# Kernel optimization log

Hardware: AMD Instinct MI355X
Metric: run time of the kernel (lower is better)

The kernel has to match this reference:

```python
import jax, jax.numpy as jnp
import numpy as np

EPS = 1e-6  # cell eps
LN_EPS = 1e-5  # torch LayerNorm default


def layer_norm(x, gamma, beta):
    mu = jnp.mean(x, axis=-1, keepdims=True)
    var = jnp.mean(jnp.square(x - mu), axis=-1, keepdims=True)
    return (x - mu) * jax.lax.rsqrt(var + LN_EPS) * gamma + beta


def normalized_exp_gate(pre):
    centered = pre - jnp.mean(pre, axis=1, keepdims=True)
    e = jnp.exp(jnp.clip(centered, -5.0, 5.0))
    return e / (jnp.sum(e, axis=1, keepdims=True) + EPS)


def setup_inputs() -> dict:
    key = jax.random.key(0)
    B, Din, H = 8192, 512, 1024
    ks = jax.random.split(key, 16)
    std = 1.0 / np.sqrt(H)
    u = lambda k, shape: jax.random.uniform(k, shape, jnp.float32, -std, std)
    return {
        "x": jax.random.normal(ks[0], (B, Din), jnp.float32),
        "h_prev": jax.random.normal(ks[1], (B, H), jnp.float32),
        "c_prev": jax.random.normal(ks[2], (B, H), jnp.float32),
        "Wx": u(ks[3], (4 * H, Din)),
        "bx": u(ks[4], (4 * H,)),
        "Wh": u(ks[5], (4 * H, H)),
        "bh": u(ks[6], (4 * H,)),
        "ln_in_g": u(ks[7], (4 * H,)),
        "ln_in_b": u(ks[8], (4 * H,)),
        "ln_hu_g": u(ks[9], (4 * H,)),
        "ln_hu_b": u(ks[10], (4 * H,)),
        "ln_c_g": u(ks[11], (H,)),
        "ln_c_b": u(ks[12], (H,)),
        "ln_h_g": u(ks[13], (H,)),
        "ln_h_b": u(ks[14], (H,)),
    }


def reference(x, h_prev, c_prev, Wx, bx, Wh, bh,
              ln_in_g, ln_in_b, ln_hu_g, ln_hu_b,
              ln_c_g, ln_c_b, ln_h_g, ln_h_b):
    # dropout p=0 -> identity (eval mode)
    gates_x = layer_norm(x @ Wx.T + bx, ln_in_g, ln_in_b)      # [B, 4H]
    gates_h = layer_norm(h_prev @ Wh.T + bh, ln_hu_g, ln_hu_b)  # [B, 4H]
    gates = gates_x + gates_h
    i, f, g, o = jnp.split(gates, 4, axis=1)
    i = normalized_exp_gate(i)
    f = normalized_exp_gate(f)
    gate_sum = i + f
    i = i / (gate_sum + EPS)
    f = f / (gate_sum + EPS)
    c_tilde = jnp.tanh(g)
    c = layer_norm(f * c_prev + i * c_tilde, ln_c_g, ln_c_b)
    o = jax.nn.sigmoid(o)
    c_out = layer_norm(jnp.tanh(c), ln_h_g, ln_h_b)
    h = o * c_out
    return (h, c)
```

## Files before the change

### kernel.cpp

```cpp
#include <hip/hip_runtime.h>
#include <hip/hip_bf16.h>
#include <stdint.h>
#include <math.h>

#define EPS_CELL 1e-6f
#define LN_EPS   1e-5f

typedef short short8 __attribute__((ext_vector_type(8)));
typedef float f32x4 __attribute__((ext_vector_type(4)));
typedef unsigned short ushort;

__device__ __forceinline__ ushort f2bf(float f) {
    union { float f; uint32_t u; } v; v.f = f;
    uint32_t r = v.u + 0x7FFFu + ((v.u >> 16) & 1u);
    return (ushort)(r >> 16);
}
__device__ __forceinline__ float bfbits2f(uint32_t hi16_in_place) {
    union { uint32_t u; float f; } v; v.u = hi16_in_place;
    return v.f;
}

__device__ __forceinline__ float fexp(float x)  { return __builtin_amdgcn_exp2f(x * 1.4426950408889634f); }
__device__ __forceinline__ float frcp(float x)  { return __builtin_amdgcn_rcpf(x); }
__device__ __forceinline__ float frsq(float x)  { return __builtin_amdgcn_rsqf(x); }
__device__ __forceinline__ float ftanh(float x) {
    float xc = fminf(fmaxf(x, -15.f), 15.f);
    float t  = fexp(2.f * xc);
    return (t - 1.f) * frcp(t + 1.f);
}
__device__ __forceinline__ float fsigm(float x) { return frcp(1.f + fexp(-x)); }

__global__ __launch_bounds__(256) void cast_all(
        const float* __restrict__ x,  const float* __restrict__ h,
        const float* __restrict__ wx, const float* __restrict__ wh,
        ushort* __restrict__ xb, ushort* __restrict__ hb,
        ushort* __restrict__ wxb, ushort* __restrict__ whb) {
    long i = ((long)blockIdx.x * 256 + threadIdx.x) * 8;
    const float* src; ushort* dst; long off;
    if      (i <  4194304L) { src = x;  dst = xb;  off = i; }
    else if (i < 12582912L) { src = h;  dst = hb;  off = i - 4194304L; }
    else if (i < 14680064L) { src = wx; dst = wxb; off = i - 12582912L; }
    else                    { src = wh; dst = whb; off = i - 14680064L; }
    const float4* p = (const float4*)(src + off);
    float4 a = p[0], b = p[1];
    uint4 r;
    r.x = (uint32_t)f2bf(a.x) | ((uint32_t)f2bf(a.y) << 16);
    r.y = (uint32_t)f2bf(a.z) | ((uint32_t)f2bf(a.w) << 16);
    r.z = (uint32_t)f2bf(b.x) | ((uint32_t)f2bf(b.y) << 16);
    r.w = (uint32_t)f2bf(b.z) | ((uint32_t)f2bf(b.w) << 16);
    *(uint4*)(dst + off) = r;
}

#define BAR()        __builtin_amdgcn_s_barrier()
#define SPRIO(x)     __builtin_amdgcn_s_setprio(x)
#define WAIT_LGKM0() do { asm volatile("s_waitcnt lgkmcnt(0)" ::: "memory"); \
                          __builtin_amdgcn_sched_barrier(0); } while (0)
#define WAIT_VM6()   do { asm volatile("s_waitcnt vmcnt(6)" ::: "memory"); \
                          __builtin_amdgcn_sched_barrier(0); } while (0)
#define WAIT_VM0()   do { asm volatile("s_waitcnt vmcnt(0)" ::: "memory"); \
                          __builtin_amdgcn_sched_barrier(0); } while (0)

template<int K>
__global__ __launch_bounds__(512, 2) void gemm256_8ph(
        const ushort* __restrict__ Ag,
        const ushort* __restrict__ Bg,
        const float*  __restrict__ bias,
        ushort* __restrict__ C,
        int GN, int m_base) {
    constexpr int NT = K / 64;
    constexpr int NP = NT / 2;

    __shared__ ushort lds[65536];

    const int t    = threadIdx.x;
    const int lane = t & 63;
    const int w    = t >> 6;
    const int wr   = w >> 2;
    const int wc   = w & 3;
    const int ln   = lane & 15;
    const int hi   = lane >> 4;
    const int sx   = ln & 7;

    const int bid = blockIdx.x;
    const int cpx = gridDim.x >> 3;
    const int wg  = (bid & 7) * cpx + (bid >> 3);
    const int n0  = (wg & 15) * 256;
    const int m0  = (wg >> 4) * 256 + m_base;

    const int trow = t >> 3;
    const int scol = (((t & 7) ^ (trow & 7)) * 8);

#define STG_A(buf, j, kb) __builtin_amdgcn_global_load_lds( \
    (const __attribute__((address_space(1))) void*)(Ag + (size_t)(m0 + (j)*64 + trow) * K + (kb) + scol), \
    (__attribute__((address_space(3))) void*)(lds + (buf)*32768 + (j)*4096 + t*8), 16, 0, 0)
#define STG_B(buf, j, kb) __builtin_amdgcn_global_load_lds( \
    (const __attribute__((address_space(1))) void*)(Bg + (size_t)(n0 + (j)*64 + trow) * K + (kb) + scol), \
    (__attribute__((address_space(3))) void*)(lds + (buf)*32768 + 16384 + (j)*4096 + t*8), 16, 0, 0)

    const int ca0  = ((0 + hi) ^ sx) * 8;
    const int ca1  = ((4 + hi) ^ sx) * 8;
    const int arow = (wr * 16 + ln) * 64;
    const int brow = (wc * 16 + ln) * 64 + 16384;

    short8 af[2][4], bf0[2][2], bf1[2][2];
    f32x4  acc[8][4] = {};

#define LD_A(buf, mbase) do { _Pragma("unroll") for (int m = 0; m < 4; ++m) { \
    af[0][m] = *(const short8*)&lds[(buf)*32768 + arow + ((mbase)+m)*2048 + ca0]; \
    af[1][m] = *(const short8*)&lds[(buf)*32768 + arow + ((mbase)+m)*2048 + ca1]; } } while (0)
#define LD_B(dst, buf, nbase) do { _Pragma("unroll") for (int n = 0; n < 2; ++n) { \
    dst[0][n] = *(const short8*)&lds[(buf)*32768 + brow + ((nbase)+n)*4096 + ca0]; \
    dst[1][n] = *(const short8*)&lds[(buf)*32768 + brow + ((nbase)+n)*4096 + ca1]; } } while (0)
#define MMQ(mb, nb, B_) do { _Pragma("unroll") for (int kk = 0; kk < 2; ++kk) \
    _Pragma("unroll") for (int m = 0; m < 4; ++m) \
    _Pragma("unroll") for (int n = 0; n < 2; ++n) \
        acc[(mb)+m][(nb)+n] = __builtin_amdgcn_mfma_f32_16x16x32_bf16( \
            af[kk][m], B_[kk][n], acc[(mb)+m][(nb)+n], 0, 0, 0); } while (0)

    STG_B(0,0,0);  STG_B(0,1,0);
    STG_A(0,0,0);  STG_A(0,1,0);
    STG_B(0,2,0);  STG_B(0,3,0);
    STG_A(0,2,0);  STG_A(0,3,0);
    STG_B(1,0,64); STG_B(1,1,64);
    STG_A(1,0,64); STG_A(1,1,64);
    STG_B(1,2,64); STG_B(1,3,64);
    WAIT_VM6(); BAR();

    for (int p = 0; p < NP; ++p) {
        const int k1 = (2*p + 1) * 64;
        const int t2 = (2*p + 2 < NT) ? (2*p + 2) : (2*p);
        const int t3 = (2*p + 3 < NT) ? (2*p + 3) : (2*p + 1);
        const int k2 = t2 * 64, k3 = t3 * 64;

        LD_A(0, 0); LD_B(bf0, 0, 0);
        STG_A(1,2,k1); STG_A(1,3,k1);
        BAR(); WAIT_LGKM0();
        SPRIO(1); MMQ(0,0,bf0); SPRIO(0); BAR();
        LD_B(bf1, 0, 2);
        STG_B(0,0,k2); STG_B(0,1,k2);
        BAR(); WAIT_LGKM0();
        SPRIO(1); MMQ(0,2,bf1); SPRIO(0); BAR();
        LD_A(0, 4);
        STG_A(0,0,k2); STG_A(0,1,k2);
        BAR(); WAIT_LGKM0();
        SPRIO(1); MMQ(4,0,bf0); SPRIO(0); BAR();
        STG_B(0,2,k2); STG_B(0,3,k2);
        BAR();
        SPRIO(1); MMQ(4,2,bf1); SPRIO(0);
        WAIT_VM6(); BAR();
        LD_A(1, 0); LD_B(bf0, 1, 0);
        STG_A(0,2,k2); STG_A(0,3,k2);
        BAR(); WAIT_LGKM0();
        SPRIO(1); MMQ(0,0,bf0); SPRIO(0); BAR();
        LD_B(bf1, 1, 2);
        STG_B(1,0,k3); STG_B(1,1,k3);
        BAR(); WAIT_LGKM0();
        SPRIO(1); MMQ(0,2,bf1); SPRIO(0); BAR();
        LD_A(1, 4);
        STG_A(1,0,k3); STG_A(1,1,k3);
        BAR(); WAIT_LGKM0();
        SPRIO(1); MMQ(4,0,bf0); SPRIO(0); BAR();
        STG_B(1,2,k3); STG_B(1,3,k3);
        BAR();
        SPRIO(1); MMQ(4,2,bf1); SPRIO(0);
        WAIT_VM6(); BAR();
    }

    WAIT_VM0();
    BAR();
#pragma unroll
    for (int n = 0; n < 4; ++n) {
        int cl   = n * 64 + wc * 16 + ln;
        float bv = bias[n0 + cl];
#pragma unroll
        for (int m = 0; m < 8; ++m) {
#pragma unroll
            for (int r = 0; r < 4; ++r) {
                int row = m * 32 + wr * 16 + hi * 4 + r;
                int sc  = (cl & 7) + ((((cl >> 3) ^ (row & 7))) << 3);
                lds[row * 256 + sc] = f2bf(acc[m][n][r] + bv);
            }
        }
    }
    BAR();
    {
        const int rr = t >> 5;
        const int oc = (t & 31) * 8;
#pragma unroll
        for (int i = 0; i < 16; ++i) {
            int row = i * 16 + rr;
            int sc  = (((oc >> 3) ^ (row & 7)) << 3);
            uint4 vv = *(const uint4*)&lds[row * 256 + sc];
            *(uint4*)(C + (size_t)(m0 + row) * GN + n0 + oc) = vv;
        }
    }
#undef STG_A
#undef STG_B
#undef LD_A
#undef LD_B
#undef MMQ
}

template<int NV>
__device__ __forceinline__ void reduce2(float* v0, float* v1, float* s0, float* s1) {
    const int lane = threadIdx.x & 63;
    const int w    = threadIdx.x >> 6;
#pragma unroll
    for (int i = 0; i < NV; ++i) {
        float a = v0[i], b = v1[i];
#pragma unroll
        for (int m = 32; m > 0; m >>= 1) {
            a += __shfl_xor(a, m, 64);
            b += __shfl_xor(b, m, 64);
        }
        if (lane == 0) { s0[i * 4 + w] = a; s1[i * 4 + w] = b; }
    }
    __syncthreads();
#pragma unroll
    for (int i = 0; i < NV; ++i) {
        v0[i] = s0[i * 4 + 0] + s0[i * 4 + 1] + s0[i * 4 + 2] + s0[i * 4 + 3];
        v1[i] = s1[i * 4 + 0] + s1[i * 4 + 1] + s1[i * 4 + 2] + s1[i * 4 + 3];
    }
}

__global__ __launch_bounds__(256) void fused_cell2(
        const ushort* __restrict__ U, const ushort* __restrict__ V,
        const float* __restrict__ c_prev,
        const float* __restrict__ g_in, const float* __restrict__ b_in,
        const float* __restrict__ g_hu, const float* __restrict__ b_hu,
        const float* __restrict__ g_c,  const float* __restrict__ b_c,
        const float* __restrict__ g_h,  const float* __restrict__ b_h,
        float* __restrict__ out_h, float* __restrict__ out_c) {
    __shared__ float sred[2][4][16];
    const int t  = threadIdx.x;
    const int c0 = t * 4;
    const int rb = blockIdx.x * 2;

    uint2 uu[2][4], vv[2][4];
    float4 cp4[2];
#pragma unroll
    for (int rj = 0; rj < 2; ++rj) {
        const size_t rowG = (size_t)(rb + rj) * 4096;
#pragma unroll
        for (int q = 0; q < 4; ++q) {
            uu[rj][q] = *(const uint2*)(U + rowG + q * 1024 + c0);
            vv[rj][q] = *(const uint2*)(V + rowG + q * 1024 + c0);
        }
        cp4[rj] = *(const float4*)(c_prev + (size_t)(rb + rj) * 1024 + c0);
    }
    float4 gc4 = *(const float4*)(g_c + c0);
    float4 bc4 = *(const float4*)(b_c + c0);
    float4 gh4 = *(const float4*)(g_h + c0);
    float4 bh4 = *(const float4*)(b_h + c0);

    float red0[4] = {0.f, 0.f, 0.f, 0.f};
    float red1[4] = {0.f, 0.f, 0.f, 0.f};
#pragma unroll
    for (int rj = 0; rj < 2; ++rj) {
        float* rd = rj ? red1 : red0;
#pragma unroll
        for (int q = 0; q < 4; ++q) {
            float u0 = bfbits2f(uu[rj][q].x << 16), u1 = bfbits2f(uu[rj][q].x & 0xFFFF0000u);
            float u2 = bfbits2f(uu[rj][q].y << 16), u3 = bfbits2f(uu[rj][q].y & 0xFFFF0000u);
            float v0 = bfbits2f(vv[rj][q].x << 16), v1 = bfbits2f(vv[rj][q].x & 0xFFFF0000u);
            float v2 = bfbits2f(vv[rj][q].y << 16), v3 = bfbits2f(vv[rj][q].y & 0xFFFF0000u);
            rd[0] += u0 + u1 + u2 + u3;
            rd[1] += u0 * u0 + u1 * u1 + u2 * u2 + u3 * u3;
            rd[2] += v0 + v1 + v2 + v3;
            rd[3] += v0 * v0 + v1 * v1 + v2 * v2 + v3 * v3;
        }
    }
    reduce2<4>(red0, red1, sred[0][0], sred[1][0]);
    const float inv4096 = 1.f / 4096.f;
    float mu_u[2], rs_u[2], mu_v[2], rs_v[2];
    mu_u[0] = red0[0] * inv4096; mu_v[0] = red0[2] * inv4096;
    rs_u[0] = frsq(red0[1] * inv4096 - mu_u[0] * mu_u[0] + LN_EPS);
    rs_v[0] = frsq(red0[3] * inv4096 - mu_v[0] * mu_v[0] + LN_EPS);
    mu_u[1] = red1[0] * inv4096; mu_v[1] = red1[2] * inv4096;
    rs_u[1] = frsq(red1[1] * inv4096 - mu_u[1] * mu_u[1] + LN_EPS);
    rs_v[1] = frsq(red1[3] * inv4096 - mu_v[1] * mu_v[1] + LN_EPS);

    float gate[2][4][4];
#pragma unroll
    for (int q = 0; q < 4; ++q) {
        const int idx = q * 1024 + c0;
        float4 ga = *(const float4*)(g_in + idx);
        float4 ba = *(const float4*)(b_in + idx);
        float4 gb = *(const float4*)(g_hu + idx);
        float4 bb = *(const float4*)(b_hu + idx);
        float gaa[4] = {ga.x, ga.y, ga.z, ga.w};
        float baa[4] = {ba.x, ba.y, ba.z, ba.w};
        float gba[4] = {gb.x, gb.y, gb.z, gb.w};
        float bba[4] = {bb.x, bb.y, bb.z, bb.w};
#pragma unroll
        for (int rj = 0; rj < 2; ++rj) {
            float uf[4], vf[4];
            uf[0] = bfbits2f(uu[rj][q].x << 16); uf[1] = bfbits2f(uu[rj][q].x & 0xFFFF0000u);
            uf[2] = bfbits2f(uu[rj][q].y << 16); uf[3] = bfbits2f(uu[rj][q].y & 0xFFFF0000u);
            vf[0] = bfbits2f(vv[rj][q].x << 16); vf[1] = bfbits2f(vv[rj][q].x & 0xFFFF0000u);
            vf[2] = bfbits2f(vv[rj][q].y << 16); vf[3] = bfbits2f(vv[rj][q].y & 0xFFFF0000u);
#pragma unroll
            for (int j = 0; j < 4; ++j) {
                float zu = (uf[j] - mu_u[rj]) * rs_u[rj];
                float zv = (vf[j] - mu_v[rj]) * rs_v[rj];
                gate[rj][q][j] = zu * gaa[j] + baa[j] + zv * gba[j] + bba[j];
            }
        }
    }

    float ei[2][4], ef[2][4];
    red0[0] = red0[1] = red1[0] = red1[1] = 0.f;
#pragma unroll
    for (int rj = 0; rj < 2; ++rj) {
        float* rd = rj ? red1 : red0;
#pragma unroll
        for (int q = 0; q < 4; ++q) {
            ei[rj][q] = fexp(fminf(fmaxf(gate[rj][0][q], -20.f), 20.f));
            ef[rj][q] = fexp(fminf(fmaxf(gate[rj][1][q], -20.f), 20.f));
            rd[0] += ei[rj][q]; rd[1] += ef[rj][q];
        }
    }
    reduce2<2>(red0, red1, sred[0][1], sred[1][1]);
    float inv_si[2], inv_sf[2];
    inv_si[0] = frcp(red0[0] + EPS_CELL); inv_sf[0] = frcp(red0[1] + EPS_CELL);
    inv_si[1] = frcp(red1[0] + EPS_CELL); inv_sf[1] = frcp(red1[1] + EPS_CELL);

    float cpv[2][4];
    red0[0] = red0[1] = red1[0] = red1[1] = 0.f;
#pragma unroll
    for (int rj = 0; rj < 2; ++rj) {
        float* rd = rj ? red1 : red0;
        float cpr[4] = {cp4[rj].x, cp4[rj].y, cp4[rj].z, cp4[rj].w};
#pragma unroll
        for (int q = 0; q < 4; ++q) {
            float in_ = ei[rj][q] * inv_si[rj];
            float fn_ = ef[rj][q] * inv_sf[rj];
            float den = frcp(in_ + fn_ + EPS_CELL);
            cpv[rj][q] = fn_ * den * cpr[q] + in_ * den * ftanh(gate[rj][2][q]);
            rd[0] += cpv[rj][q]; rd[1] += cpv[rj][q] * cpv[rj][q];
        }
    }
    reduce2<2>(red0, red1, sred[0][2], sred[1][2]);
    const float inv1024 = 1.f / 1024.f;
    float mu_c[2], rs_c[2];
    mu_c[0] = red0[0] * inv1024;
    rs_c[0] = frsq(red0[1] * inv1024 - mu_c[0] * mu_c[0] + LN_EPS);
    mu_c[1] = red1[0] * inv1024;
    rs_c[1] = frsq(red1[1] * inv1024 - mu_c[1] * mu_c[1] + LN_EPS);

    float th[2][4];
    {
        float gca[4] = {gc4.x, gc4.y, gc4.z, gc4.w};
        float bca[4] = {bc4.x, bc4.y, bc4.z, bc4.w};
        red0[0] = red0[1] = red1[0] = red1[1] = 0.f;
#pragma unroll
        for (int rj = 0; rj < 2; ++rj) {
            float* rd = rj ? red1 : red0;
            float cv[4];
#pragma unroll
            for (int q = 0; q < 4; ++q) {
                cv[q] = (cpv[rj][q] - mu_c[rj]) * rs_c[rj] * gca[q] + bca[q];
                th[rj][q] = ftanh(cv[q]);
                rd[0] += th[rj][q]; rd[1] += th[rj][q] * th[rj][q];
            }
            float4 o; o.x = cv[0]; o.y = cv[1]; o.z = cv[2]; o.w = cv[3];
            *(float4*)(out_c + (size_t)(rb + rj) * 1024 + c0) = o;
        }
    }
    reduce2<2>(red0, red1, sred[0][3], sred[1][3]);
    float mu_t[2], rs_t[2];
    mu_t[0] = red0[0] * inv1024;
    rs_t[0] = frsq(red0[1] * inv1024 - mu_t[0] * mu_t[0] + LN_EPS);
    mu_t[1] = red1[0] * inv1024;
    rs_t[1] = frsq(red1[1] * inv1024 - mu_t[1] * mu_t[1] + LN_EPS);

    {
        float gha[4] = {gh4.x, gh4.y, gh4.z, gh4.w};
        float bha[4] = {bh4.x, bh4.y, bh4.z, bh4.w};
#pragma unroll
        for (int rj = 0; rj < 2; ++rj) {
            float hv[4];
#pragma unroll
            for (int q = 0; q < 4; ++q) {
                float co = (th[rj][q] - mu_t[rj]) * rs_t[rj] * gha[q] + bha[q];
                hv[q] = fsigm(gate[rj][3][q]) * co;
            }
            float4 o; o.x = hv[0]; o.y = hv[1]; o.z = hv[2]; o.w = hv[3];
            *(float4*)(out_h + (size_t)(rb + rj) * 1024 + c0) = o;
        }
    }
}

extern "C" void kernel_launch(void* const* d_in, const int* in_sizes, int n_in,
                              void* d_out, int out_size, void* d_ws, size_t ws_size,
                              hipStream_t stream) {
    const float* x       = (const float*)d_in[0];
    const float* h_prev  = (const float*)d_in[1];
    const float* c_prev  = (const float*)d_in[2];
    const float* Wx      = (const float*)d_in[3];
    const float* bx      = (const float*)d_in[4];
    const float* Wh      = (const float*)d_in[5];
    const float* bh      = (const float*)d_in[6];
    const float* ln_in_g = (const float*)d_in[7];
    const float* ln_in_b = (const float*)d_in[8];
    const float* ln_hu_g = (const float*)d_in[9];
    const float* ln_hu_b = (const float*)d_in[10];
    const float* ln_c_g  = (const float*)d_in[11];
    const float* ln_c_b  = (const float*)d_in[12];
    const float* ln_h_g  = (const float*)d_in[13];
    const float* ln_h_b  = (const float*)d_in[14];

    const int B = 8192, Din = 512, H = 1024, G = 4096;

    ushort* xb  = (ushort*)d_ws;
    ushort* hb  = xb  + (size_t)B * Din;
    ushort* wxb = hb  + (size_t)B * H;
    ushort* whb = wxb + (size_t)G * Din;
    ushort* U   = whb + (size_t)G * H;
    ushort* V   = U   + (size_t)B * G;

    cast_all<<<9216, 256, 0, stream>>>(x, h_prev, Wx, Wh, xb, hb, wxb, whb);

    gemm256_8ph<512> <<<dim3(256), 512, 0, stream>>>(xb, wxb, bx, U, G, 0);
    gemm256_8ph<512> <<<dim3(256), 512, 0, stream>>>(xb, wxb, bx, U, G, 4096);
    gemm256_8ph<1024><<<dim3(256), 512, 0, stream>>>(hb, whb, bh, V, G, 0);
    gemm256_8ph<1024><<<dim3(256), 512, 0, stream>>>(hb, whb, bh, V, G, 4096);

    float* out_h = (float*)d_out;
    float* out_c = out_h + (size_t)B * H;
    fused_cell2<<<B / 2, 256, 0, stream>>>(U, V, c_prev,
                                           ln_in_g, ln_in_b, ln_hu_g, ln_hu_b,
                                           ln_c_g, ln_c_b, ln_h_g, ln_h_b,
                                           out_h, out_c);
}
```

Before: 213.9 us.

## Make fused cell kernel persistent over row pairs with register double-buffered prefetch

The fused LayerNorm/gate kernel now has each block process four consecutive row pairs instead of one. It loads the next pair's U, V and c_prev values into a second register buffer while the current pair is computed. The aim is to hide global-memory latency behind the reduction and transcendental work, and to load the per-column LN parameters once per block. In exchange the kernel uses more registers, which may lower occupancy, and the grid shrinks from 4096 blocks to 1024.

```diff
diff --git a/kernel.cpp b/kernel.cpp
--- a/kernel.cpp
+++ b/kernel.cpp
@@ -223,7 +223,7 @@
     }
 }
 
-__global__ __launch_bounds__(256) void fused_cell2(
+__global__ __launch_bounds__(256) void fused_cell_p(
         const ushort* __restrict__ U, const ushort* __restrict__ V,
         const float* __restrict__ c_prev,
         const float* __restrict__ g_in, const float* __restrict__ b_in,
@@ -234,159 +234,181 @@
     __shared__ float sred[2][4][16];
     const int t  = threadIdx.x;
     const int c0 = t * 4;
-    const int rb = blockIdx.x * 2;
-
-    uint2 uu[2][4], vv[2][4];
-    float4 cp4[2];
+    const int pb = blockIdx.x * 4;
+
+    const float4 gc4 = *(const float4*)(g_c + c0);
+    const float4 bc4 = *(const float4*)(b_c + c0);
+    const float4 gh4 = *(const float4*)(g_h + c0);
+    const float4 bh4 = *(const float4*)(b_h + c0);
+
+    uint2 uu[2][2][4], vv[2][2][4];
+    float4 cp[2][2];
+
 #pragma unroll
     for (int rj = 0; rj < 2; ++rj) {
-        const size_t rowG = (size_t)(rb + rj) * 4096;
+        const size_t rowG = (size_t)(2 * pb + rj) * 4096;
 #pragma unroll
         for (int q = 0; q < 4; ++q) {
-            uu[rj][q] = *(const uint2*)(U + rowG + q * 1024 + c0);
-            vv[rj][q] = *(const uint2*)(V + rowG + q * 1024 + c0);
-        }
-        cp4[rj] = *(const float4*)(c_prev + (size_t)(rb + rj) * 1024 + c0);
-    }
-    float4 gc4 = *(const float4*)(g_c + c0);
-    float4 bc4 = *(const float4*)(b_c + c0);
-    float4 gh4 = *(const float4*)(g_h + c0);
-    float4 bh4 = *(const float4*)(b_h + c0);
-
-    float red0[4] = {0.f, 0.f, 0.f, 0.f};
-    float red1[4] = {0.f, 0.f, 0.f, 0.f};
-#pragma unroll
-    for (int rj = 0; rj < 2; ++rj) {
-        float* rd = rj ? red1 : red0;
-#pragma unroll
-        for (int q = 0; q < 4; ++q) {
-            float u0 = bfbits2f(uu[rj][q].x << 16), u1 = bfbits2f(uu[rj][q].x & 0xFFFF0000u);
-            float u2 = bfbits2f(uu[rj][q].y << 16), u3 = bfbits2f(uu[rj][q].y & 0xFFFF0000u);
-            float v0 = bfbits2f(vv[rj][q].x << 16), v1 = bfbits2f(vv[rj][q].x & 0xFFFF0000u);
-            float v2 = bfbits2f(vv[rj][q].y << 16), v3 = bfbits2f(vv[rj][q].y & 0xFFFF0000u);
-            rd[0] += u0 + u1 + u2 + u3;
-            rd[1] += u0 * u0 + u1 * u1 + u2 * u2 + u3 * u3;
-            rd[2] += v0 + v1 + v2 + v3;
-            rd[3] += v0 * v0 + v1 * v1 + v2 * v2 + v3 * v3;
-        }
-    }
-    reduce2<4>(red0, red1, sred[0][0], sred[1][0]);
-    const float inv4096 = 1.f / 4096.f;
-    float mu_u[2], rs_u[2], mu_v[2], rs_v[2];
-    mu_u[0] = red0[0] * inv4096; mu_v[0] = red0[2] * inv4096;
-    rs_u[0] = frsq(red0[1] * inv4096 - mu_u[0] * mu_u[0] + LN_EPS);
-    rs_v[0] = frsq(red0[3] * inv4096 - mu_v[0] * mu_v[0] + LN_EPS);
-    mu_u[1] = red1[0] * inv4096; mu_v[1] = red1[2] * inv4096;
-    rs_u[1] = frsq(red1[1] * inv4096 - mu_u[1] * mu_u[1] + LN_EPS);
-    rs_v[1] = frsq(red1[3] * inv4096 - mu_v[1] * mu_v[1] + LN_EPS);
-
-    float gate[2][4][4];
-#pragma unroll
-    for (int q = 0; q < 4; ++q) {
-        const int idx = q * 1024 + c0;
-        float4 ga = *(const float4*)(g_in + idx);
-        float4 ba = *(const float4*)(b_in + idx);
-        float4 gb = *(const float4*)(g_hu + idx);
-        float4 bb = *(const float4*)(b_hu + idx);
-        float gaa[4] = {ga.x, ga.y, ga.z, ga.w};
-        float baa[4] = {ba.x, ba.y, ba.z, ba.w};
-        float gba[4] = {gb.x, gb.y, gb.z, gb.w};
-        float bba[4] = {bb.x, bb.y, bb.z, bb.w};
-#pragma unroll
-        for (int rj = 0; rj < 2; ++rj) {
-            float uf[4], vf[4];
-            uf[0] = bfbits2f(uu[rj][q].x << 16); uf[1] = bfbits2f(uu[rj][q].x & 0xFFFF0000u);
-            uf[2] = bfbits2f(uu[rj][q].y << 16); uf[3] = bfbits2f(uu[rj][q].y & 0xFFFF0000u);
-            vf[0] = bfbits2f(vv[rj][q].x << 16); vf[1] = bfbits2f(vv[rj][q].x & 0xFFFF0000u);
-            vf[2] = bfbits2f(vv[rj][q].y << 16); vf[3] = bfbits2f(vv[rj][q].y & 0xFFFF0000u);
-#pragma unroll
-            for (int j = 0; j < 4; ++j) {
-                float zu = (uf[j] - mu_u[rj]) * rs_u[rj];
-                float zv = (vf[j] - mu_v[rj]) * rs_v[rj];
-                gate[rj][q][j] = zu * gaa[j] + baa[j] + zv * gba[j] + bba[j];
-            }
-        }
-    }
-
-    float ei[2][4], ef[2][4];
-    red0[0] = red0[1] = red1[0] = red1[1] = 0.f;
-#pragma unroll
-    for (int rj = 0; rj < 2; ++rj) {
-        float* rd = rj ? red1 : red0;
-#pragma unroll
-        for (int q = 0; q < 4; ++q) {
-            ei[rj][q] = fexp(fminf(fmaxf(gate[rj][0][q], -20.f), 20.f));
-            ef[rj][q] = fexp(fminf(fmaxf(gate[rj][1][q], -20.f), 20.f));
-            rd[0] += ei[rj][q]; rd[1] += ef[rj][q];
-        }
-    }
-    reduce2<2>(red0, red1, sred[0][1], sred[1][1]);
-    float inv_si[2], inv_sf[2];
-    inv_si[0] = frcp(red0[0] + EPS_CELL); inv_sf[0] = frcp(red0[1] + EPS_CELL);
-    inv_si[1] = frcp(red1[0] + EPS_CELL); inv_sf[1] = frcp(red1[1] + EPS_CELL);
-
-    float cpv[2][4];
-    red0[0] = red0[1] = red1[0] = red1[1] = 0.f;
-#pragma unroll
-    for (int rj = 0; rj < 2; ++rj) {
-        float* rd = rj ? red1 : red0;
-        float cpr[4] = {cp4[rj].x, cp4[rj].y, cp4[rj].z, cp4[rj].w};
-#pragma unroll
-        for (int q = 0; q < 4; ++q) {
-            float in_ = ei[rj][q] * inv_si[rj];
-            float fn_ = ef[rj][q] * inv_sf[rj];
-            float den = frcp(in_ + fn_ + EPS_CELL);
-            cpv[rj][q] = fn_ * den * cpr[q] + in_ * den * ftanh(gate[rj][2][q]);
-            rd[0] += cpv[rj][q]; rd[1] += cpv[rj][q] * cpv[rj][q];
-        }
-    }
-    reduce2<2>(red0, red1, sred[0][2], sred[1][2]);
-    const float inv1024 = 1.f / 1024.f;
-    float mu_c[2], rs_c[2];
-    mu_c[0] = red0[0] * inv1024;
-    rs_c[0] = frsq(red0[1] * inv1024 - mu_c[0] * mu_c[0] + LN_EPS);
-    mu_c[1] = red1[0] * inv1024;
-    rs_c[1] = frsq(red1[1] * inv1024 - mu_c[1] * mu_c[1] + LN_EPS);
-
-    float th[2][4];
-    {
-        float gca[4] = {gc4.x, gc4.y, gc4.z, gc4.w};
-        float bca[4] = {bc4.x, bc4.y, bc4.z, bc4.w};
-        red0[0] = red0[1] = red1[0] = red1[1] = 0.f;
+            uu[0][rj][q] = *(const uint2*)(U + rowG + q * 1024 + c0);
+            vv[0][rj][q] = *(const uint2*)(V + rowG + q * 1024 + c0);
+        }
+        cp[0][rj] = *(const float4*)(c_prev + (size_t)(2 * pb + rj) * 1024 + c0);
+    }
+
+#pragma unroll
+    for (int p = 0; p < 4; ++p) {
+        const int cur = p & 1, nxt = cur ^ 1;
+        const int rb = 2 * (pb + p);
+
+        if (p < 3) {
+            const int rn = 2 * (pb + p + 1);
+#pragma unroll
+            for (int rj = 0; rj < 2; ++rj) {
+                const size_t rowG = (size_t)(rn + rj) * 4096;
+#pragma unroll
+                for (int q = 0; q < 4; ++q) {
+                    uu[nxt][rj][q] = *(const uint2*)(U + rowG + q * 1024 + c0);
+                    vv[nxt][rj][q] = *(const uint2*)(V + rowG + q * 1024 + c0);
+                }
+                cp[nxt][rj] = *(const float4*)(c_prev + (size_t)(rn + rj) * 1024 + c0);
+            }
+        }
+
+        float red0[4] = {0.f, 0.f, 0.f, 0.f};
+        float red1[4] = {0.f, 0.f, 0.f, 0.f};
 #pragma unroll
         for (int rj = 0; rj < 2; ++rj) {
             float* rd = rj ? red1 : red0;
-            float cv[4];
 #pragma unroll
             for (int q = 0; q < 4; ++q) {
-                cv[q] = (cpv[rj][q] - mu_c[rj]) * rs_c[rj] * gca[q] + bca[q];
-                th[rj][q] = ftanh(cv[q]);
-                rd[0] += th[rj][q]; rd[1] += th[rj][q] * th[rj][q];
-            }
-            float4 o; o.x = cv[0]; o.y = cv[1]; o.z = cv[2]; o.w = cv[3];
-            *(float4*)(out_c + (size_t)(rb + rj) * 1024 + c0) = o;
-        }
-    }
-    reduce2<2>(red0, red1, sred[0][3], sred[1][3]);
-    float mu_t[2], rs_t[2];
-    mu_t[0] = red0[0] * inv1024;
-    rs_t[0] = frsq(red0[1] * inv1024 - mu_t[0] * mu_t[0] + LN_EPS);
-    mu_t[1] = red1[0] * inv1024;
-    rs_t[1] = frsq(red1[1] * inv1024 - mu_t[1] * mu_t[1] + LN_EPS);
-
-    {
-        float gha[4] = {gh4.x, gh4.y, gh4.z, gh4.w};
-        float bha[4] = {bh4.x, bh4.y, bh4.z, bh4.w};
+                float u0 = bfbits2f(uu[cur][rj][q].x << 16), u1 = bfbits2f(uu[cur][rj][q].x & 0xFFFF0000u);
+                float u2 = bfbits2f(uu[cur][rj][q].y << 16), u3 = bfbits2f(uu[cur][rj][q].y & 0xFFFF0000u);
+                float v0 = bfbits2f(vv[cur][rj][q].x << 16), v1 = bfbits2f(vv[cur][rj][q].x & 0xFFFF0000u);
+                float v2 = bfbits2f(vv[cur][rj][q].y << 16), v3 = bfbits2f(vv[cur][rj][q].y & 0xFFFF0000u);
+                rd[0] += u0 + u1 + u2 + u3;
+                rd[1] += u0 * u0 + u1 * u1 + u2 * u2 + u3 * u3;
+                rd[2] += v0 + v1 + v2 + v3;
+                rd[3] += v0 * v0 + v1 * v1 + v2 * v2 + v3 * v3;
+            }
+        }
+        reduce2<4>(red0, red1, sred[0][0], sred[1][0]);
+        const float inv4096 = 1.f / 4096.f;
+        float mu_u[2], rs_u[2], mu_v[2], rs_v[2];
+        mu_u[0] = red0[0] * inv4096; mu_v[0] = red0[2] * inv4096;
+        rs_u[0] = frsq(red0[1] * inv4096 - mu_u[0] * mu_u[0] + LN_EPS);
+        rs_v[0] = frsq(red0[3] * inv4096 - mu_v[0] * mu_v[0] + LN_EPS);
+        mu_u[1] = red1[0] * inv4096; mu_v[1] = red1[2] * inv4096;
+        rs_u[1] = frsq(red1[1] * inv4096 - mu_u[1] * mu_u[1] + LN_EPS);
+        rs_v[1] = frsq(red1[3] * inv4096 - mu_v[1] * mu_v[1] + LN_EPS);
+
+        float gate[2][4][4];
+#pragma unroll
+        for (int q = 0; q < 4; ++q) {
+            const int idx = q * 1024 + c0;
+            float4 ga = *(const float4*)(g_in + idx);
+            float4 ba = *(const float4*)(b_in + idx);
+            float4 gb = *(const float4*)(g_hu + idx);
+            float4 bb = *(const float4*)(b_hu + idx);
+            float gaa[4] = {ga.x, ga.y, ga.z, ga.w};
+            float baa[4] = {ba.x, ba.y, ba.z, ba.w};
+            float gba[4] = {gb.x, gb.y, gb.z, gb.w};
+            float bba[4] = {bb.x, bb.y, bb.z, bb.w};
+#pragma unroll
+            for (int rj = 0; rj < 2; ++rj) {
+                float uf[4], vf[4];
+                uf[0] = bfbits2f(uu[cur][rj][q].x << 16); uf[1] = bfbits2f(uu[cur][rj][q].x & 0xFFFF0000u);
+                uf[2] = bfbits2f(uu[cur][rj][q].y << 16); uf[3] = bfbits2f(uu[cur][rj][q].y & 0xFFFF0000u);
+                vf[0] = bfbits2f(vv[cur][rj][q].x << 16); vf[1] = bfbits2f(vv[cur][rj][q].x & 0xFFFF0000u);
+                vf[2] = bfbits2f(vv[cur][rj][q].y << 16); vf[3] = bfbits2f(vv[cur][rj][q].y & 0xFFFF0000u);
+#pragma unroll
+                for (int j = 0; j < 4; ++j) {
+                    float zu = (uf[j] - mu_u[rj]) * rs_u[rj];
+                    float zv = (vf[j] - mu_v[rj]) * rs_v[rj];
+                    gate[rj][q][j] = zu * gaa[j] + baa[j] + zv * gba[j] + bba[j];
+                }
+            }
+        }
+
+        float ei[2][4], ef[2][4];
+        red0[0] = red0[1] = red1[0] = red1[1] = 0.f;
 #pragma unroll
         for (int rj = 0; rj < 2; ++rj) {
-            float hv[4];
+            float* rd = rj ? red1 : red0;
 #pragma unroll
             for (int q = 0; q < 4; ++q) {
-                float co = (th[rj][q] - mu_t[rj]) * rs_t[rj] * gha[q] + bha[q];
-                hv[q] = fsigm(gate[rj][3][q]) * co;
-            }
-            float4 o; o.x = hv[0]; o.y = hv[1]; o.z = hv[2]; o.w = hv[3];
-            *(float4*)(out_h + (size_t)(rb + rj) * 1024 + c0) = o;
+                ei[rj][q] = fexp(fminf(fmaxf(gate[rj][0][q], -20.f), 20.f));
+                ef[rj][q] = fexp(fminf(fmaxf(gate[rj][1][q], -20.f), 20.f));
+                rd[0] += ei[rj][q]; rd[1] += ef[rj][q];
+            }
+        }
+        reduce2<2>(red0, red1, sred[0][1], sred[1][1]);
+        float inv_si[2], inv_sf[2];
+        inv_si[0] = frcp(red0[0] + EPS_CELL); inv_sf[0] = frcp(red0[1] + EPS_CELL);
+        inv_si[1] = frcp(red1[0] + EPS_CELL); inv_sf[1] = frcp(red1[1] + EPS_CELL);
+
+        float cpv[2][4];
+        red0[0] = red0[1] = red1[0] = red1[1] = 0.f;
+#pragma unroll
+        for (int rj = 0; rj < 2; ++rj) {
+            float* rd = rj ? red1 : red0;
+            float cpr[4] = {cp[cur][rj].x, cp[cur][rj].y, cp[cur][rj].z, cp[cur][rj].w};
+#pragma unroll
+            for (int q = 0; q < 4; ++q) {
+                float in_ = ei[rj][q] * inv_si[rj];
+                float fn_ = ef[rj][q] * inv_sf[rj];
+                float den = frcp(in_ + fn_ + EPS_CELL);
+                cpv[rj][q] = fn_ * den * cpr[q] + in_ * den * ftanh(gate[rj][2][q]);
+                rd[0] += cpv[rj][q]; rd[1] += cpv[rj][q] * cpv[rj][q];
+            }
+        }
+        reduce2<2>(red0, red1, sred[0][2], sred[1][2]);
+        const float inv1024 = 1.f / 1024.f;
+        float mu_c[2], rs_c[2];
+        mu_c[0] = red0[0] * inv1024;
+        rs_c[0] = frsq(red0[1] * inv1024 - mu_c[0] * mu_c[0] + LN_EPS);
+        mu_c[1] = red1[0] * inv1024;
+        rs_c[1] = frsq(red1[1] * inv1024 - mu_c[1] * mu_c[1] + LN_EPS);
+
+        float th[2][4];
+        {
+            float gca[4] = {gc4.x, gc4.y, gc4.z, gc4.w};
+            float bca[4] = {bc4.x, bc4.y, bc4.z, bc4.w};
+            red0[0] = red0[1] = red1[0] = red1[1] = 0.f;
+#pragma unroll
+            for (int rj = 0; rj < 2; ++rj) {
+                float* rd = rj ? red1 : red0;
+                float cv[4];
+#pragma unroll
+                for (int q = 0; q < 4; ++q) {
+                    cv[q] = (cpv[rj][q] - mu_c[rj]) * rs_c[rj] * gca[q] + bca[q];
+                    th[rj][q] = ftanh(cv[q]);
+                    rd[0] += th[rj][q]; rd[1] += th[rj][q] * th[rj][q];
+                }
+                float4 o; o.x = cv[0]; o.y = cv[1]; o.z = cv[2]; o.w = cv[3];
+                *(float4*)(out_c + (size_t)(rb + rj) * 1024 + c0) = o;
+            }
+        }
+        reduce2<2>(red0, red1, sred[0][3], sred[1][3]);
+        float mu_t[2], rs_t[2];
+        mu_t[0] = red0[0] * inv1024;
+        rs_t[0] = frsq(red0[1] * inv1024 - mu_t[0] * mu_t[0] + LN_EPS);
+        mu_t[1] = red1[0] * inv1024;
+        rs_t[1] = frsq(red1[1] * inv1024 - mu_t[1] * mu_t[1] + LN_EPS);
+
+        {
+            float gha[4] = {gh4.x, gh4.y, gh4.z, gh4.w};
+            float bha[4] = {bh4.x, bh4.y, bh4.z, bh4.w};
+#pragma unroll
+            for (int rj = 0; rj < 2; ++rj) {
+                float hv[4];
+#pragma unroll
+                for (int q = 0; q < 4; ++q) {
+                    float co = (th[rj][q] - mu_t[rj]) * rs_t[rj] * gha[q] + bha[q];
+                    hv[q] = fsigm(gate[rj][3][q]) * co;
+                }
+                float4 o; o.x = hv[0]; o.y = hv[1]; o.z = hv[2]; o.w = hv[3];
+                *(float4*)(out_h + (size_t)(rb + rj) * 1024 + c0) = o;
+            }
         }
     }
 }
@@ -428,7 +450,7 @@
 
     float* out_h = (float*)d_out;
     float* out_c = out_h + (size_t)B * H;
-    fused_cell2<<<B / 2, 256, 0, stream>>>(U, V, c_prev,
+    fused_cell_p<<<1024, 256, 0, stream>>>(U, V, c_prev,
                                            ln_in_g, ln_in_b, ln_hu_g, ln_hu_b,
                                            ln_c_g, ln_c_b, ln_h_g, ln_h_b,
                                            out_h, out_c);
```

Result: slower. 224.0 us (+4.7%).
